# Performance work log

Hardware: AMD Instinct MI355X
Metric: run time of the kernel (lower is better)

## Reference

```python
import jax, jax.numpy as jnp
import numpy as np
import math

B, S, D, E, H = 8, 384, 768, 768, 12
HD = E // H
MAXL = 512

def _xavier(key, shape):
    fan_in, fan_out = shape[1], shape[0]
    lim = math.sqrt(6.0 / (fan_in + fan_out))
    return jax.random.uniform(key, shape, jnp.float32, -lim, lim)

def setup_inputs() -> dict:
    key = jax.random.key(0)
    ks = jax.random.split(key, 12)
    return {
        "x": jax.random.normal(ks[0], (B, S, D), jnp.float32),
        "mask": jnp.ones((B, S), jnp.int32),
        "segment_ids": jax.random.randint(ks[1], (B, S), 0, 2).astype(jnp.int32),
        "sep_distances": jax.random.normal(ks[2], (B, S), jnp.float32),
        "Wq": _xavier(ks[3], (E, D)), "bq": jnp.zeros((E,), jnp.float32),
        "Wk": _xavier(ks[4], (E, D)), "bk": jnp.zeros((E,), jnp.float32),
        "Wv": _xavier(ks[5], (E, D)), "bv": jnp.zeros((E,), jnp.float32),
        "rel_emb": jax.random.normal(ks[6], (2 * MAXL - 1, D), jnp.float32),
        "Wpk": _xavier(ks[7], (E, D)), "bpk": jnp.zeros((E,), jnp.float32),
        "Wpq": _xavier(ks[8], (E, D)), "bpq": jnp.zeros((E,), jnp.float32),
        "same_bias": jnp.zeros((H,), jnp.float32),
        "cross_bias": jnp.zeros((H,), jnp.float32),
        "sep_scale": jnp.full((H,), 0.25, jnp.float32),
        "sep_decay": jnp.full((H,), 0.35, jnp.float32),
        "Wo": _xavier(ks[9], (D, E)), "bo": jnp.zeros((D,), jnp.float32),
    }

def reference(x, mask, segment_ids, sep_distances, Wq, bq, Wk, bk, Wv, bv,
              rel_emb, Wpk, bpk, Wpq, bpq, same_bias, cross_bias,
              sep_scale, sep_decay, Wo, bo):
    b, s, _ = x.shape
    def shape_heads(t):  # [b,s,E] -> [b,H,s,HD]
        return t.reshape(b, s, H, HD).transpose(0, 2, 1, 3)
    q = shape_heads(x @ Wq.T + bq)
    k = shape_heads(x @ Wk.T + bk)
    v = shape_heads(x @ Wv.T + bv)
    # relative positions i - j, clamped and shifted
    rel_pos = jnp.arange(s)[:, None] - jnp.arange(s)[None, :]
    rel_pos = jnp.clip(rel_pos, -(MAXL - 1), MAXL - 1) + (MAXL - 1)
    rel = rel_emb[rel_pos]                     # [s,s,D]
    pos_k = (rel @ Wpk.T + bpk).reshape(s, s, H, HD)  # [i,j,h,d]
    pos_q = (rel @ Wpq.T + bpq).reshape(s, s, H, HD)
    c2c = jnp.einsum('bhid,bhjd->bhij', q, k)
    c2p = jnp.einsum('bhid,ijhd->bhij', q, pos_k)
    p2c = jnp.einsum('ijhd,bhjd->bhij', pos_q, k)
    logits = (c2c + c2p + p2c) / math.sqrt(HD * 3.0)
    # segment bias
    same = (segment_ids[:, :, None] == segment_ids[:, None, :]).astype(jnp.float32)[:, None]  # [b,1,s,s]
    cross = 1.0 - same
    hb = lambda p: p[None, :, None, None]
    seg_bias = same * hb(same_bias) + cross * hb(cross_bias)
    abs_sep = jnp.abs(sep_distances)
    gap = jnp.abs(abs_sep[:, :, None] - abs_sep[:, None, :])[:, None]  # [b,1,s,s]
    decay = jax.nn.softplus(sep_decay)[None, :, None, None] + 1e-4
    seg_bias = seg_bias + cross * jnp.exp(-gap * decay) * hb(sep_scale)
    logits = logits + seg_bias
    # mask: [b,s] -> [b,1,1,s]
    m = mask[:, None, None, :]
    logits = jnp.where(m == 0, jnp.float32(-9e15), logits)
    attn = jax.nn.softmax(logits, axis=-1)
    vals = jnp.einsum('bhij,bhjd->bhid', attn, v)
    vals = vals.transpose(0, 2, 1, 3).reshape(b, s, E)
    return vals @ Wo.T + bo
```

## Files before the change

kernel.cpp:

```cpp
#include <hip/hip_runtime.h>
#include <math.h>

#define B_  8
#define S_  384
#define H_  12
#define HD_ 64
#define E_  768
#define D_  768

typedef float  floatx4 __attribute__((ext_vector_type(4)));
typedef __bf16 bf16x8  __attribute__((ext_vector_type(8)));
typedef unsigned int ux4 __attribute__((ext_vector_type(4)));

__device__ __forceinline__ unsigned short f2bf(float f) {
    union { float f; unsigned u; } x; x.f = f;
    unsigned r = x.u + 0x7fff + ((x.u >> 16) & 1);
    return (unsigned short)(r >> 16);
}
__device__ __forceinline__ float bf2f(unsigned short u) {
    union { unsigned u; float f; } x; x.u = ((unsigned)u) << 16;
    return x.f;
}
__device__ __forceinline__ bf16x8 gld8(const unsigned short* p) {
    return __builtin_bit_cast(bf16x8, *(const ux4*)p);
}
__device__ __forceinline__ int tadr(int row, int cD) {
    return (row * 8 + (cD ^ (row & 7))) * 8;
}
__device__ __forceinline__ bf16x8 lds8(const unsigned short* base, int row, int cD) {
    return __builtin_bit_cast(bf16x8, *(const ux4*)(base + tadr(row, cD)));
}

__global__ __launch_bounds__(256) void convert_all(
    const float* __restrict__ x,
    const float* __restrict__ Wq, const float* __restrict__ Wk,
    const float* __restrict__ Wv, const float* __restrict__ Wo,
    const float* __restrict__ Wpk, const float* __restrict__ Wpq,
    const float* __restrict__ rel128,
    unsigned short* __restrict__ xb,
    unsigned short* __restrict__ wqb, unsigned short* __restrict__ wkb,
    unsigned short* __restrict__ wvb, unsigned short* __restrict__ wob,
    unsigned short* __restrict__ wpkb, unsigned short* __restrict__ wpqb,
    unsigned short* __restrict__ relb)
{
    const int seg = blockIdx.y;
    const int e = (blockIdx.x * 256 + threadIdx.x) * 4;
    const float* src;
    unsigned short* dst;
    if (seg < 4)       { src = x + (size_t)seg * 589824; dst = xb + (size_t)seg * 589824; }
    else if (seg == 4) { src = Wq;  dst = wqb; }
    else if (seg == 5) { src = Wk;  dst = wkb; }
    else if (seg == 6) { src = Wv;  dst = wvb; }
    else if (seg == 7) { src = Wo;  dst = wob; }
    else if (seg == 8) { src = Wpk; dst = wpkb; }
    else if (seg == 9) { src = Wpq; dst = wpqb; }
    else               { src = rel128; dst = relb; }

    float4 v;
    if (seg == 10 && e >= 767 * 768) v = make_float4(0.f, 0.f, 0.f, 0.f);
    else                             v = *(const float4*)(src + e);
    ushort4 o;
    o.x = f2bf(v.x); o.y = f2bf(v.y); o.z = f2bf(v.z); o.w = f2bf(v.w);
    *(ushort4*)(dst + e) = o;
}

__global__ __launch_bounds__(256) void proj_all(
    const unsigned short* __restrict__ xb, const unsigned short* __restrict__ relb,
    const unsigned short* __restrict__ wq, const unsigned short* __restrict__ wk,
    const unsigned short* __restrict__ wv, const unsigned short* __restrict__ wpk,
    const unsigned short* __restrict__ wpq,
    const float* __restrict__ bq, const float* __restrict__ bk,
    const float* __restrict__ bv, const float* __restrict__ bpk,
    const float* __restrict__ bpq,
    unsigned short* __restrict__ qb, unsigned short* __restrict__ kb,
    unsigned short* __restrict__ vtb, unsigned short* __restrict__ pkb,
    unsigned short* __restrict__ pqb)
{
    const int bid = blockIdx.x;
    int z, mt, nt;
    if (bid < 864) {
        z = bid / 288; const int r = bid - z * 288; mt = r / 6; nt = r - mt * 6;
    } else {
        const int r2 = bid - 864; z = 3 + r2 / 72;
        const int r = r2 % 72; mt = r / 6; nt = r - mt * 6;
    }
    const int m0 = mt * 64, n0 = nt * 128;

    const unsigned short* A = (z < 3) ? xb : relb;
    const unsigned short* W = (z == 0) ? wq : (z == 1) ? wk : (z == 2) ? wv
                            : (z == 3) ? wpk : wpq;
    const float* bias = (z == 0) ? bq : (z == 1) ? bk : (z == 2) ? bv
                      : (z == 3) ? bpk : bpq;
    unsigned short* C = (z == 0) ? qb : (z == 1) ? kb : (z == 2) ? vtb
                      : (z == 3) ? pkb : pqb;

    __shared__ unsigned short As[64 * 64];
    __shared__ unsigned short Ws[128 * 64];

    const int tid  = threadIdx.x;
    const int lane = tid & 63;
    const int wv_  = tid >> 6;
    const int quad = lane >> 4, l16 = lane & 15;

    floatx4 acc[4][2];
#pragma unroll
    for (int i = 0; i < 4; ++i)
#pragma unroll
        for (int j = 0; j < 2; ++j) acc[i][j] = (floatx4){0.f, 0.f, 0.f, 0.f};

    for (int k0 = 0; k0 < 768; k0 += 64) {
        __syncthreads();
#pragma unroll
        for (int r = 0; r < 2; ++r) {
            const int idx = tid + 256 * r;
            const int row = idx >> 3, cL = idx & 7, cD = cL ^ (row & 7);
            __builtin_amdgcn_global_load_lds(
                (__attribute__((address_space(1))) void*)(A + (size_t)(m0 + row) * 768 + k0 + cD * 8),
                (__attribute__((address_space(3))) void*)&As[idx * 8], 16, 0, 0);
        }
#pragma unroll
        for (int r = 0; r < 4; ++r) {
            const int idx = tid + 256 * r;
            const int row = idx >> 3, cL = idx & 7, cD = cL ^ (row & 7);
            __builtin_amdgcn_global_load_lds(
                (__attribute__((address_space(1))) void*)(W + (size_t)(n0 + row) * 768 + k0 + cD * 8),
                (__attribute__((address_space(3))) void*)&Ws[idx * 8], 16, 0, 0);
        }
        __syncthreads();

        bf16x8 a[4][2], b[2][2];
#pragma unroll
        for (int mi = 0; mi < 4; ++mi)
#pragma unroll
            for (int kc = 0; kc < 2; ++kc)
                a[mi][kc] = lds8(As, mi * 16 + l16, kc * 4 + quad);
#pragma unroll
        for (int ni = 0; ni < 2; ++ni)
#pragma unroll
            for (int kc = 0; kc < 2; ++kc)
                b[ni][kc] = lds8(Ws, wv_ * 32 + ni * 16 + l16, kc * 4 + quad);
#pragma unroll
        for (int mi = 0; mi < 4; ++mi)
#pragma unroll
            for (int ni = 0; ni < 2; ++ni)
#pragma unroll
                for (int kc = 0; kc < 2; ++kc)
                    acc[mi][ni] = __builtin_amdgcn_mfma_f32_16x16x32_bf16(
                        a[mi][kc], b[ni][kc], acc[mi][ni], 0, 0, 0);
    }

#pragma unroll
    for (int ni = 0; ni < 2; ++ni) {
        const int n = n0 + wv_ * 32 + ni * 16 + l16;
        const float bn = bias[n];
#pragma unroll
        for (int mi = 0; mi < 4; ++mi) {
            const int mbase = m0 + mi * 16 + quad * 4;
            if (z == 2) {
                const int bb = mbase / S_, s = mbase - bb * S_;
                const int h = n >> 6, hd = n & 63;
                ushort4 o;
                o.x = f2bf(acc[mi][ni][0] + bn);
                o.y = f2bf(acc[mi][ni][1] + bn);
                o.z = f2bf(acc[mi][ni][2] + bn);
                o.w = f2bf(acc[mi][ni][3] + bn);
                *(ushort4*)&C[(((size_t)(bb * H_ + h) << 6) + hd) * S_ + s] = o;
            } else if (z < 2) {
#pragma unroll
                for (int reg = 0; reg < 4; ++reg) {
                    const int m = mbase + reg;
                    const int bb = m / S_, s = m - bb * S_;
                    const int h = n >> 6, hd = n & 63;
                    C[(((size_t)(bb * H_ + h) * S_ + s) << 6) + hd] =
                        f2bf(acc[mi][ni][reg] + bn);
                }
            } else {
#pragma unroll
                for (int reg = 0; reg < 4; ++reg)
                    C[(size_t)(mbase + reg) * 768 + n] = f2bf(acc[mi][ni][reg] + bn);
            }
        }
    }
}

__global__ __launch_bounds__(256) void gemm_out(
    const unsigned short* __restrict__ A, const unsigned short* __restrict__ W,
    const float* __restrict__ bias, float* __restrict__ C)
{
    const int bid = blockIdx.x;
    const int kb = bid & 1;
    const int t  = bid >> 1;
    const int mt = t / 6, nt = t - mt * 6;
    const int m0 = mt * 64, n0 = nt * 128;

    __shared__ unsigned short As[64 * 64];
    __shared__ unsigned short Ws[128 * 64];

    const int tid  = threadIdx.x;
    const int lane = tid & 63;
    const int wv_  = tid >> 6;
    const int quad = lane >> 4, l16 = lane & 15;

    floatx4 acc[4][2];
#pragma unroll
    for (int i = 0; i < 4; ++i)
#pragma unroll
        for (int j = 0; j < 2; ++j) acc[i][j] = (floatx4){0.f, 0.f, 0.f, 0.f};

    const int kbeg = kb * 384, kend = kbeg + 384;
    for (int k0 = kbeg; k0 < kend; k0 += 64) {
        __syncthreads();
#pragma unroll
        for (int r = 0; r < 2; ++r) {
            const int idx = tid + 256 * r;
            const int row = idx >> 3, cL = idx & 7, cD = cL ^ (row & 7);
            __builtin_amdgcn_global_load_lds(
                (__attribute__((address_space(1))) void*)(A + (size_t)(m0 + row) * 768 + k0 + cD * 8),
                (__attribute__((address_space(3))) void*)&As[idx * 8], 16, 0, 0);
        }
#pragma unroll
        for (int r = 0; r < 4; ++r) {
            const int idx = tid + 256 * r;
            const int row = idx >> 3, cL = idx & 7, cD = cL ^ (row & 7);
            __builtin_amdgcn_global_load_lds(
                (__attribute__((address_space(1))) void*)(W + (size_t)(n0 + row) * 768 + k0 + cD * 8),
                (__attribute__((address_space(3))) void*)&Ws[idx * 8], 16, 0, 0);
        }
        __syncthreads();

        bf16x8 a[4][2], b[2][2];
#pragma unroll
        for (int mi = 0; mi < 4; ++mi)
#pragma unroll
            for (int kc = 0; kc < 2; ++kc)
                a[mi][kc] = lds8(As, mi * 16 + l16, kc * 4 + quad);
#pragma unroll
        for (int ni = 0; ni < 2; ++ni)
#pragma unroll
            for (int kc = 0; kc < 2; ++kc)
                b[ni][kc] = lds8(Ws, wv_ * 32 + ni * 16 + l16, kc * 4 + quad);
#pragma unroll
        for (int mi = 0; mi < 4; ++mi)
#pragma unroll
            for (int ni = 0; ni < 2; ++ni)
#pragma unroll
                for (int kc = 0; kc < 2; ++kc)
                    acc[mi][ni] = __builtin_amdgcn_mfma_f32_16x16x32_bf16(
                        a[mi][kc], b[ni][kc], acc[mi][ni], 0, 0, 0);
    }

#pragma unroll
    for (int ni = 0; ni < 2; ++ni) {
        const int n = n0 + wv_ * 32 + ni * 16 + l16;
        const float bn = (kb == 0) ? bias[n] : 0.f;
#pragma unroll
        for (int mi = 0; mi < 4; ++mi)
#pragma unroll
            for (int reg = 0; reg < 4; ++reg) {
                const int m = m0 + mi * 16 + quad * 4 + reg;
                atomicAdd(&C[(size_t)m * 768 + n], acc[mi][ni][reg] + bn);
            }
    }
}

__global__ __launch_bounds__(256, 3) void attn_mfma(
    const unsigned short* __restrict__ qg, const unsigned short* __restrict__ kg,
    const unsigned short* __restrict__ vtg,
    const unsigned short* __restrict__ pkg, const unsigned short* __restrict__ pqg,
    const int* __restrict__ seg, const float* __restrict__ sep,
    const int* __restrict__ mask,
    const float* __restrict__ same_bias, const float* __restrict__ cross_bias,
    const float* __restrict__ sep_scale, const float* __restrict__ sep_decay,
    unsigned short* __restrict__ part_O, float* __restrict__ part_ml)
{
    __shared__ unsigned short PKs[128 * 64];
    __shared__ unsigned short PQs[128 * 64];
    __shared__ float CP[64 * 68];

    const int tid  = threadIdx.x;
    const int lane = tid & 63, w = tid >> 6;
    const int l16  = lane & 15, quad = lane >> 4;
    const int it = blockIdx.x, h = blockIdx.y;
    const int b  = blockIdx.z / 6, jt = blockIdx.z - 6 * b;
    const int i0 = it * 64, j0 = jt * 64;
    const size_t bh = (size_t)(b * H_ + h);

    const unsigned short* kbase  = kg  + bh * S_ * 64;
    const unsigned short* vtbase = vtg + bh * 64 * S_;
    const int dbase = i0 - j0 + 320;

#pragma unroll
    for (int r = 0; r < 4; ++r) {
        const int idx = tid + 256 * r;
        const int srow = idx >> 3, cL = idx & 7, cD = cL ^ (srow & 7);
        const size_t go = (size_t)(dbase + srow) * 768 + h * 64 + cD * 8;
        __builtin_amdgcn_global_load_lds(
            (__attribute__((address_space(1))) void*)(pkg + go),
            (__attribute__((address_space(3))) void*)&PKs[idx * 8], 16, 0, 0);
        __builtin_amdgcn_global_load_lds(
            (__attribute__((address_space(1))) void*)(pqg + go),
            (__attribute__((address_space(3))) void*)&PQs[idx * 8], 16, 0, 0);
    }

    bf16x8 qf[2];
#pragma unroll
    for (int ks = 0; ks < 2; ++ks)
        qf[ks] = gld8(qg + (bh * S_ + i0 + 16 * w + l16) * 64 + ks * 32 + quad * 8);

    bf16x8 kf[4][2];
#pragma unroll
    for (int nj = 0; nj < 4; ++nj)
#pragma unroll
        for (int ks = 0; ks < 2; ++ks)
            kf[nj][ks] = gld8(kbase + (size_t)(j0 + 16 * nj + l16) * 64
                              + ks * 32 + quad * 8);

    bf16x8 vtf[4][2];
#pragma unroll
    for (int nd = 0; nd < 4; ++nd)
#pragma unroll
        for (int ks = 0; ks < 2; ++ks)
            vtf[nd][ks] = gld8(vtbase + (size_t)(16 * nd + l16) * S_
                               + j0 + ks * 32 + quad * 8);

    const int row = 16 * w + l16;
    const float aii = fabsf(sep[b * S_ + i0 + row]);
    const int   sii = seg[b * S_ + i0 + row];
    const float* sepj = sep  + b * S_ + j0;
    const int*   segj = seg  + b * S_ + j0;
    const int*   mskj = mask + b * S_ + j0;
    float ajv[16]; int sjv[16], mkv[16];
    *(float4*)&ajv[0]  = *(const float4*)&sepj[quad * 8];
    *(float4*)&ajv[4]  = *(const float4*)&sepj[quad * 8 + 4];
    *(float4*)&ajv[8]  = *(const float4*)&sepj[32 + quad * 8];
    *(float4*)&ajv[12] = *(const float4*)&sepj[32 + quad * 8 + 4];
    *(int4*)&sjv[0]  = *(const int4*)&segj[quad * 8];
    *(int4*)&sjv[4]  = *(const int4*)&segj[quad * 8 + 4];
    *(int4*)&sjv[8]  = *(const int4*)&segj[32 + quad * 8];
    *(int4*)&sjv[12] = *(const int4*)&segj[32 + quad * 8 + 4];
    *(int4*)&mkv[0]  = *(const int4*)&mskj[quad * 8];
    *(int4*)&mkv[4]  = *(const int4*)&mskj[quad * 8 + 4];
    *(int4*)&mkv[8]  = *(const int4*)&mskj[32 + quad * 8];
    *(int4*)&mkv[12] = *(const int4*)&mskj[32 + quad * 8 + 4];

    const float sb  = same_bias[h];
    const float cb  = cross_bias[h];
    const float ssc = sep_scale[h];
    const float sd  = sep_decay[h];
    const float dec = fmaxf(sd, 0.f) + log1pf(__expf(-fabsf(sd))) + 1e-4f;
    const float isc = 0.07216878364870323f;

    float biasv[16]; unsigned mkbits = 0;
#pragma unroll
    for (int e = 0; e < 16; ++e) {
        const float gap = fabsf(aii - fabsf(ajv[e]));
        biasv[e] = (sii == sjv[e]) ? sb : cb + __expf(-gap * dec) * ssc;
        mkbits |= (mkv[e] != 0 ? 1u : 0u) << e;
    }

#pragma unroll
    for (int nj = 0; nj < 4; ++nj) {
        floatx4 acc = (floatx4){0.f, 0.f, 0.f, 0.f};
#pragma unroll
        for (int ks = 0; ks < 2; ++ks)
            acc = __builtin_amdgcn_mfma_f32_16x16x32_bf16(qf[ks], kf[nj][ks], acc, 0, 0, 0);
#pragma unroll
        for (int reg = 0; reg < 4; ++reg) {
            const int ii = 16 * w + quad * 4 + reg;
            CP[ii * 68 + 16 * nj + l16] = acc[reg];
        }
    }

    __syncthreads();

#pragma unroll
    for (int f = 0; f < 5; ++f) {
        const int nd = w + f;
        floatx4 acc = (floatx4){0.f, 0.f, 0.f, 0.f};
#pragma unroll
        for (int ks = 0; ks < 2; ++ks) {
            bf16x8 bf = lds8(PKs, 16 * nd + l16, ks * 4 + quad);
            acc = __builtin_amdgcn_mfma_f32_16x16x32_bf16(qf[ks], bf, acc, 0, 0, 0);
        }
        const int ddloc = 16 * nd + l16;
#pragma unroll
        for (int reg = 0; reg < 4; ++reg) {
            const int ii = 16 * w + quad * 4 + reg;
            const int jj = ii - ddloc + 63;
            if (jj >= 0 && jj < 64)
                CP[ii * 68 + jj] += acc[reg];
        }
    }

#pragma unroll
    for (int f = 0; f < 5; ++f) {
        const int nd = w + f;
        bf16x8 pqf[2];
#pragma unroll
        for (int ks = 0; ks < 2; ++ks)
            pqf[ks] = lds8(PQs, 16 * nd + l16, ks * 4 + quad);
#pragma unroll
        for (int g = 0; g < 2; ++g) {
            const int nj = (g == 0) ? (3 - f) : (4 - f);
            if (nj < 0 || nj > 3) continue;
            floatx4 acc = (floatx4){0.f, 0.f, 0.f, 0.f};
#pragma unroll
            for (int ks = 0; ks < 2; ++ks)
                acc = __builtin_amdgcn_mfma_f32_16x16x32_bf16(pqf[ks], kf[nj][ks], acc, 0, 0, 0);
            const int jj = 16 * nj + l16;
#pragma unroll
            for (int reg = 0; reg < 4; ++reg) {
                const int ddloc = 16 * nd + quad * 4 + reg;
                const int ii = ddloc + jj - 63;
                if (ii >= 16 * w && ii < 16 * w + 16)
                    CP[ii * 68 + jj] += acc[reg];
            }
        }
    }

    floatx4 cp0 = *(const floatx4*)&CP[row * 68 + quad * 8];
    floatx4 cp1 = *(const floatx4*)&CP[row * 68 + quad * 8 + 4];
    floatx4 cp2 = *(const floatx4*)&CP[row * 68 + 32 + quad * 8];
    floatx4 cp3 = *(const floatx4*)&CP[row * 68 + 32 + quad * 8 + 4];

    float lg[16];
    float tmax = -INFINITY;
#pragma unroll
    for (int e = 0; e < 16; ++e) {
        const float cpv = (e < 4) ? cp0[e] : (e < 8) ? cp1[e - 4]
                        : (e < 12) ? cp2[e - 8] : cp3[e - 12];
        float xv = cpv * isc + biasv[e];
        if (!((mkbits >> e) & 1u)) xv = -9.0e15f;
        lg[e] = xv;
        tmax = fmaxf(tmax, xv);
    }
    tmax = fmaxf(tmax, __shfl_xor(tmax, 16));
    tmax = fmaxf(tmax, __shfl_xor(tmax, 32));

    float rs = 0.f;
    unsigned int pk32[8];
#pragma unroll
    for (int e = 0; e < 8; ++e) {
        const float e0 = __expf(lg[2 * e]     - tmax);
        const float e1 = __expf(lg[2 * e + 1] - tmax);
        rs += e0 + e1;
        pk32[e] = (unsigned)f2bf(e0) | ((unsigned)f2bf(e1) << 16);
    }
    rs += __shfl_xor(rs, 16);
    rs += __shfl_xor(rs, 32);

    float* pml = part_ml + (size_t)(jt * 576 + ((b * H_ + h) * 6 + it)) * 128;
    if (quad == 0) {
        pml[row]      = tmax;
        pml[64 + row] = rs;
    }

    bf16x8 pA[2];
    pA[0] = __builtin_bit_cast(bf16x8, (ux4){pk32[0], pk32[1], pk32[2], pk32[3]});
    pA[1] = __builtin_bit_cast(bf16x8, (ux4){pk32[4], pk32[5], pk32[6], pk32[7]});
    floatx4 O[4];
#pragma unroll
    for (int nd = 0; nd < 4; ++nd) {
        O[nd] = (floatx4){0.f, 0.f, 0.f, 0.f};
#pragma unroll
        for (int ks = 0; ks < 2; ++ks)
            O[nd] = __builtin_amdgcn_mfma_f32_16x16x32_bf16(pA[ks], vtf[nd][ks], O[nd], 0, 0, 0);
    }

    unsigned short* pO = part_O + (size_t)(jt * 576 + ((b * H_ + h) * 6 + it)) * 4096;
#pragma unroll
    for (int nd = 0; nd < 4; ++nd) {
        const int d = 16 * nd + l16;
#pragma unroll
        for (int reg = 0; reg < 4; ++reg) {
            const int ii = 16 * w + quad * 4 + reg;
            pO[ii * 64 + d] = f2bf(O[nd][reg]);
        }
    }
}

__global__ __launch_bounds__(256) void merge_attn(
    const unsigned short* __restrict__ part_O, const float* __restrict__ part_ml,
    unsigned short* __restrict__ vals)
{
    const int idx = blockIdx.x;
    const int b  = idx / (H_ * 6);
    const int r  = idx - b * H_ * 6;
    const int h  = r / 6, it = r - h * 6;
    const int tid = threadIdx.x;
    const int ii = tid >> 2, c = (tid & 3) * 16;

    float m[6], l[6];
#pragma unroll
    for (int jc = 0; jc < 6; ++jc) {
        const float* pml = part_ml + (size_t)(jc * 576 + idx) * 128;
        m[jc] = pml[ii];
        l[jc] = pml[64 + ii];
    }
    float M = m[0];
#pragma unroll
    for (int jc = 1; jc < 6; ++jc) M = fmaxf(M, m[jc]);
    float wsum = 0.f, wc[6];
#pragma unroll
    for (int jc = 0; jc < 6; ++jc) {
        wc[jc] = __expf(m[jc] - M);
        wsum += wc[jc] * l[jc];
    }
    const float inv = (wsum > 0.f) ? 1.f / wsum : 0.f;

    float o[16];
#pragma unroll
    for (int e = 0; e < 16; ++e) o[e] = 0.f;
#pragma unroll
    for (int jc = 0; jc < 6; ++jc) {
        const unsigned short* pO = part_O + ((size_t)(jc * 576 + idx)) * 4096
                                 + ii * 64 + c;
        ux4 u0 = *(const ux4*)pO;
        ux4 u1 = *(const ux4*)(pO + 8);
        const unsigned short* us0 = (const unsigned short*)&u0;
        const unsigned short* us1 = (const unsigned short*)&u1;
#pragma unroll
        for (int e = 0; e < 8; ++e) {
            o[e]     += wc[jc] * bf2f(us0[e]);
            o[8 + e] += wc[jc] * bf2f(us1[e]);
        }
    }
    ushort4 w0, w1, w2, w3;
#pragma unroll
    for (int e = 0; e < 4; ++e) {
        ((unsigned short*)&w0)[e] = f2bf(o[e] * inv);
        ((unsigned short*)&w1)[e] = f2bf(o[4 + e] * inv);
        ((unsigned short*)&w2)[e] = f2bf(o[8 + e] * inv);
        ((unsigned short*)&w3)[e] = f2bf(o[12 + e] * inv);
    }
    unsigned short* dst = vals + ((size_t)(b * S_ + it * 64 + ii)) * E_ + h * 64 + c;
    *(ushort4*)(dst)      = w0;
    *(ushort4*)(dst + 4)  = w1;
    *(ushort4*)(dst + 8)  = w2;
    *(ushort4*)(dst + 12) = w3;
}

extern "C" void kernel_launch(void* const* d_in, const int* in_sizes, int n_in,
                              void* d_out, int out_size, void* d_ws, size_t ws_size,
                              hipStream_t stream)
{
    const float* x         = (const float*)d_in[0];
    const int*   mask      = (const int*)d_in[1];
    const int*   seg       = (const int*)d_in[2];
    const float* sep       = (const float*)d_in[3];
    const float* Wq        = (const float*)d_in[4];
    const float* bq        = (const float*)d_in[5];
    const float* Wk        = (const float*)d_in[6];
    const float* bk        = (const float*)d_in[7];
    const float* Wv        = (const float*)d_in[8];
    const float* bv        = (const float*)d_in[9];
    const float* rel_emb   = (const float*)d_in[10];
    const float* Wpk       = (const float*)d_in[11];
    const float* bpk       = (const float*)d_in[12];
    const float* Wpq       = (const float*)d_in[13];
    const float* bpq       = (const float*)d_in[14];
    const float* same_bias = (const float*)d_in[15];
    const float* cross_bias= (const float*)d_in[16];
    const float* sep_scale = (const float*)d_in[17];
    const float* sep_decay = (const float*)d_in[18];
    const float* Wo        = (const float*)d_in[19];
    const float* bo        = (const float*)d_in[20];

    const size_t QKVN = (size_t)B_ * S_ * E_;
    const size_t WN   = (size_t)768 * 768;

    unsigned short* xb    = (unsigned short*)d_ws;
    unsigned short* wqb   = xb   + QKVN;
    unsigned short* wkb   = wqb  + WN;
    unsigned short* wvb   = wkb  + WN;
    unsigned short* wob   = wvb  + WN;
    unsigned short* wpkb  = wob  + WN;
    unsigned short* wpqb  = wpkb + WN;
    unsigned short* relb  = wpqb + WN;
    unsigned short* qb    = relb + WN;
    unsigned short* kb    = qb   + QKVN;
    unsigned short* vtb   = kb   + QKVN;
    unsigned short* pkb   = vtb  + QKVN;
    unsigned short* pqb   = pkb  + WN;
    unsigned short* valsb = pqb  + WN;
    unsigned short* partO = valsb + QKVN;
    float*          partml= (float*)(partO + (size_t)6 * 576 * 4096);

    hipMemsetAsync(d_out, 0, (size_t)out_size, stream);

    convert_all<<<dim3(576, 11), 256, 0, stream>>>(
        x, Wq, Wk, Wv, Wo, Wpk, Wpq, rel_emb + (size_t)128 * D_,
        xb, wqb, wkb, wvb, wob, wpkb, wpqb, relb);

    proj_all<<<dim3(1008), 256, 0, stream>>>(
        xb, relb, wqb, wkb, wvb, wpkb, wpqb,
        bq, bk, bv, bpk, bpq, qb, kb, vtb, pkb, pqb);

    attn_mfma<<<dim3(6, 12, 48), 256, 0, stream>>>(
        qb, kb, vtb, pkb, pqb, seg, sep, mask,
        same_bias, cross_bias, sep_scale, sep_decay, partO, partml);

    merge_attn<<<dim3(576), 256, 0, stream>>>(partO, partml, valsb);

    gemm_out<<<dim3(576), 256, 0, stream>>>(valsb, wob, bo, (float*)d_out);
}
```

Baseline: 210.2 us.

## Loop three key tiles per attention block with online softmax and ring-buffered position tiles

Each attention block now walks three consecutive 64-wide key tiles with an online-softmax accumulator, not one, so the split-KV factor drops from six to two. The PK/PQ relative-position tiles sit in a 128-row ring buffer in LDS, and only 64 new rows are fetched per step, so the overlapping diagonal band is reused. The merge kernel combines two partials instead of six. This cuts partial-output traffic, merge work and redundant relative-position loads. The cost is a third of the blocks (1152 vs 3456), extra syncs and loads sitting in the serial loop.

After: 239.8 us. +14.1%, slower.

```diff
diff --git a/kernel.cpp b/kernel.cpp
--- a/kernel.cpp
+++ b/kernel.cpp
@@ -281,67 +281,36 @@
     const int lane = tid & 63, w = tid >> 6;
     const int l16  = lane & 15, quad = lane >> 4;
     const int it = blockIdx.x, h = blockIdx.y;
-    const int b  = blockIdx.z / 6, jt = blockIdx.z - 6 * b;
-    const int i0 = it * 64, j0 = jt * 64;
+    const int b  = blockIdx.z >> 1, jh = blockIdx.z & 1;
+    const int i0 = it * 64;
     const size_t bh = (size_t)(b * H_ + h);
 
     const unsigned short* kbase  = kg  + bh * S_ * 64;
     const unsigned short* vtbase = vtg + bh * 64 * S_;
-    const int dbase = i0 - j0 + 320;
+    const int db0 = i0 - jh * 192 + 320;
 
 #pragma unroll
     for (int r = 0; r < 4; ++r) {
         const int idx = tid + 256 * r;
-        const int srow = idx >> 3, cL = idx & 7, cD = cL ^ (srow & 7);
-        const size_t go = (size_t)(dbase + srow) * 768 + h * 64 + cD * 8;
+        const int grow = db0 + (idx >> 3);
+        const int p = grow & 127;
+        const int cL = idx & 7, cD = cL ^ (grow & 7);
+        const size_t go = (size_t)grow * 768 + h * 64 + cD * 8;
         __builtin_amdgcn_global_load_lds(
             (__attribute__((address_space(1))) void*)(pkg + go),
-            (__attribute__((address_space(3))) void*)&PKs[idx * 8], 16, 0, 0);
+            (__attribute__((address_space(3))) void*)&PKs[(p * 8 + cL) * 8], 16, 0, 0);
         __builtin_amdgcn_global_load_lds(
             (__attribute__((address_space(1))) void*)(pqg + go),
-            (__attribute__((address_space(3))) void*)&PQs[idx * 8], 16, 0, 0);
-    }
-
+            (__attribute__((address_space(3))) void*)&PQs[(p * 8 + cL) * 8], 16, 0, 0);
+    }
+
+    const int row = 16 * w + l16;
     bf16x8 qf[2];
 #pragma unroll
     for (int ks = 0; ks < 2; ++ks)
         qf[ks] = gld8(qg + (bh * S_ + i0 + 16 * w + l16) * 64 + ks * 32 + quad * 8);
-
-    bf16x8 kf[4][2];
-#pragma unroll
-    for (int nj = 0; nj < 4; ++nj)
-#pragma unroll
-        for (int ks = 0; ks < 2; ++ks)
-            kf[nj][ks] = gld8(kbase + (size_t)(j0 + 16 * nj + l16) * 64
-                              + ks * 32 + quad * 8);
-
-    bf16x8 vtf[4][2];
-#pragma unroll
-    for (int nd = 0; nd < 4; ++nd)
-#pragma unroll
-        for (int ks = 0; ks < 2; ++ks)
-            vtf[nd][ks] = gld8(vtbase + (size_t)(16 * nd + l16) * S_
-                               + j0 + ks * 32 + quad * 8);
-
-    const int row = 16 * w + l16;
     const float aii = fabsf(sep[b * S_ + i0 + row]);
     const int   sii = seg[b * S_ + i0 + row];
-    const float* sepj = sep  + b * S_ + j0;
-    const int*   segj = seg  + b * S_ + j0;
-    const int*   mskj = mask + b * S_ + j0;
-    float ajv[16]; int sjv[16], mkv[16];
-    *(float4*)&ajv[0]  = *(const float4*)&sepj[quad * 8];
-    *(float4*)&ajv[4]  = *(const float4*)&sepj[quad * 8 + 4];
-    *(float4*)&ajv[8]  = *(const float4*)&sepj[32 + quad * 8];
-    *(float4*)&ajv[12] = *(const float4*)&sepj[32 + quad * 8 + 4];
-    *(int4*)&sjv[0]  = *(const int4*)&segj[quad * 8];
-    *(int4*)&sjv[4]  = *(const int4*)&segj[quad * 8 + 4];
-    *(int4*)&sjv[8]  = *(const int4*)&segj[32 + quad * 8];
-    *(int4*)&sjv[12] = *(const int4*)&segj[32 + quad * 8 + 4];
-    *(int4*)&mkv[0]  = *(const int4*)&mskj[quad * 8];
-    *(int4*)&mkv[4]  = *(const int4*)&mskj[quad * 8 + 4];
-    *(int4*)&mkv[8]  = *(const int4*)&mskj[32 + quad * 8];
-    *(int4*)&mkv[12] = *(const int4*)&mskj[32 + quad * 8 + 4];
 
     const float sb  = same_bias[h];
     const float cb  = cross_bias[h];
@@ -350,6 +319,38 @@
     const float dec = fmaxf(sd, 0.f) + log1pf(__expf(-fabsf(sd))) + 1e-4f;
     const float isc = 0.07216878364870323f;
 
+    bf16x8 kf[4][2], vtf[4][2];
+    float ajv[16]; int sjv[16], mkv[16];
+    {
+        const int j0 = jh * 192;
+#pragma unroll
+        for (int nj = 0; nj < 4; ++nj)
+#pragma unroll
+            for (int ks = 0; ks < 2; ++ks)
+                kf[nj][ks] = gld8(kbase + (size_t)(j0 + 16 * nj + l16) * 64
+                                  + ks * 32 + quad * 8);
+#pragma unroll
+        for (int nd = 0; nd < 4; ++nd)
+#pragma unroll
+            for (int ks = 0; ks < 2; ++ks)
+                vtf[nd][ks] = gld8(vtbase + (size_t)(16 * nd + l16) * S_
+                                   + j0 + ks * 32 + quad * 8);
+        const float* sepj = sep  + b * S_ + j0;
+        const int*   segj = seg  + b * S_ + j0;
+        const int*   mskj = mask + b * S_ + j0;
+        *(float4*)&ajv[0]  = *(const float4*)&sepj[quad * 8];
+        *(float4*)&ajv[4]  = *(const float4*)&sepj[quad * 8 + 4];
+        *(float4*)&ajv[8]  = *(const float4*)&sepj[32 + quad * 8];
+        *(float4*)&ajv[12] = *(const float4*)&sepj[32 + quad * 8 + 4];
+        *(int4*)&sjv[0]  = *(const int4*)&segj[quad * 8];
+        *(int4*)&sjv[4]  = *(const int4*)&segj[quad * 8 + 4];
+        *(int4*)&sjv[8]  = *(const int4*)&segj[32 + quad * 8];
+        *(int4*)&sjv[12] = *(const int4*)&segj[32 + quad * 8 + 4];
+        *(int4*)&mkv[0]  = *(const int4*)&mskj[quad * 8];
+        *(int4*)&mkv[4]  = *(const int4*)&mskj[quad * 8 + 4];
+        *(int4*)&mkv[8]  = *(const int4*)&mskj[32 + quad * 8];
+        *(int4*)&mkv[12] = *(const int4*)&mskj[32 + quad * 8 + 4];
+    }
     float biasv[16]; unsigned mkbits = 0;
 #pragma unroll
     for (int e = 0; e < 16; ++e) {
@@ -358,6 +359,11 @@
         mkbits |= (mkv[e] != 0 ? 1u : 0u) << e;
     }
 
+    float m_run = -INFINITY, l_run = 0.f;
+    floatx4 O[4];
+#pragma unroll
+    for (int nd = 0; nd < 4; ++nd) O[nd] = (floatx4){0.f, 0.f, 0.f, 0.f};
+
 #pragma unroll
     for (int nj = 0; nj < 4; ++nj) {
         floatx4 acc = (floatx4){0.f, 0.f, 0.f, 0.f};
@@ -374,100 +380,181 @@
     __syncthreads();
 
 #pragma unroll
-    for (int f = 0; f < 5; ++f) {
-        const int nd = w + f;
-        floatx4 acc = (floatx4){0.f, 0.f, 0.f, 0.f};
-#pragma unroll
-        for (int ks = 0; ks < 2; ++ks) {
-            bf16x8 bf = lds8(PKs, 16 * nd + l16, ks * 4 + quad);
-            acc = __builtin_amdgcn_mfma_f32_16x16x32_bf16(qf[ks], bf, acc, 0, 0, 0);
-        }
-        const int ddloc = 16 * nd + l16;
-#pragma unroll
-        for (int reg = 0; reg < 4; ++reg) {
-            const int ii = 16 * w + quad * 4 + reg;
-            const int jj = ii - ddloc + 63;
-            if (jj >= 0 && jj < 64)
-                CP[ii * 68 + jj] += acc[reg];
-        }
-    }
-
-#pragma unroll
-    for (int f = 0; f < 5; ++f) {
-        const int nd = w + f;
-        bf16x8 pqf[2];
-#pragma unroll
-        for (int ks = 0; ks < 2; ++ks)
-            pqf[ks] = lds8(PQs, 16 * nd + l16, ks * 4 + quad);
-#pragma unroll
-        for (int g = 0; g < 2; ++g) {
-            const int nj = (g == 0) ? (3 - f) : (4 - f);
-            if (nj < 0 || nj > 3) continue;
+    for (int t = 0; t < 3; ++t) {
+        const int dbt = db0 - 64 * t;
+
+#pragma unroll
+        for (int f = 0; f < 5; ++f) {
+            const int nd = w + f;
             floatx4 acc = (floatx4){0.f, 0.f, 0.f, 0.f};
 #pragma unroll
+            for (int ks = 0; ks < 2; ++ks) {
+                bf16x8 bf = lds8(PKs, (dbt + 16 * nd + l16) & 127, ks * 4 + quad);
+                acc = __builtin_amdgcn_mfma_f32_16x16x32_bf16(qf[ks], bf, acc, 0, 0, 0);
+            }
+            const int ddloc = 16 * nd + l16;
+#pragma unroll
+            for (int reg = 0; reg < 4; ++reg) {
+                const int ii = 16 * w + quad * 4 + reg;
+                const int jj = ii - ddloc + 63;
+                if (jj >= 0 && jj < 64)
+                    CP[ii * 68 + jj] += acc[reg];
+            }
+        }
+
+#pragma unroll
+        for (int f = 0; f < 5; ++f) {
+            const int nd = w + f;
+            bf16x8 pqf[2];
+#pragma unroll
             for (int ks = 0; ks < 2; ++ks)
-                acc = __builtin_amdgcn_mfma_f32_16x16x32_bf16(pqf[ks], kf[nj][ks], acc, 0, 0, 0);
-            const int jj = 16 * nj + l16;
-#pragma unroll
-            for (int reg = 0; reg < 4; ++reg) {
-                const int ddloc = 16 * nd + quad * 4 + reg;
-                const int ii = ddloc + jj - 63;
-                if (ii >= 16 * w && ii < 16 * w + 16)
-                    CP[ii * 68 + jj] += acc[reg];
-            }
-        }
-    }
-
-    floatx4 cp0 = *(const floatx4*)&CP[row * 68 + quad * 8];
-    floatx4 cp1 = *(const floatx4*)&CP[row * 68 + quad * 8 + 4];
-    floatx4 cp2 = *(const floatx4*)&CP[row * 68 + 32 + quad * 8];
-    floatx4 cp3 = *(const floatx4*)&CP[row * 68 + 32 + quad * 8 + 4];
-
-    float lg[16];
-    float tmax = -INFINITY;
-#pragma unroll
-    for (int e = 0; e < 16; ++e) {
-        const float cpv = (e < 4) ? cp0[e] : (e < 8) ? cp1[e - 4]
-                        : (e < 12) ? cp2[e - 8] : cp3[e - 12];
-        float xv = cpv * isc + biasv[e];
-        if (!((mkbits >> e) & 1u)) xv = -9.0e15f;
-        lg[e] = xv;
-        tmax = fmaxf(tmax, xv);
-    }
-    tmax = fmaxf(tmax, __shfl_xor(tmax, 16));
-    tmax = fmaxf(tmax, __shfl_xor(tmax, 32));
-
-    float rs = 0.f;
-    unsigned int pk32[8];
-#pragma unroll
-    for (int e = 0; e < 8; ++e) {
-        const float e0 = __expf(lg[2 * e]     - tmax);
-        const float e1 = __expf(lg[2 * e + 1] - tmax);
-        rs += e0 + e1;
-        pk32[e] = (unsigned)f2bf(e0) | ((unsigned)f2bf(e1) << 16);
-    }
-    rs += __shfl_xor(rs, 16);
-    rs += __shfl_xor(rs, 32);
-
-    float* pml = part_ml + (size_t)(jt * 576 + ((b * H_ + h) * 6 + it)) * 128;
-    if (quad == 0) {
-        pml[row]      = tmax;
-        pml[64 + row] = rs;
-    }
-
-    bf16x8 pA[2];
-    pA[0] = __builtin_bit_cast(bf16x8, (ux4){pk32[0], pk32[1], pk32[2], pk32[3]});
-    pA[1] = __builtin_bit_cast(bf16x8, (ux4){pk32[4], pk32[5], pk32[6], pk32[7]});
-    floatx4 O[4];
-#pragma unroll
-    for (int nd = 0; nd < 4; ++nd) {
-        O[nd] = (floatx4){0.f, 0.f, 0.f, 0.f};
-#pragma unroll
-        for (int ks = 0; ks < 2; ++ks)
-            O[nd] = __builtin_amdgcn_mfma_f32_16x16x32_bf16(pA[ks], vtf[nd][ks], O[nd], 0, 0, 0);
-    }
-
-    unsigned short* pO = part_O + (size_t)(jt * 576 + ((b * H_ + h) * 6 + it)) * 4096;
+                pqf[ks] = lds8(PQs, (dbt + 16 * nd + l16) & 127, ks * 4 + quad);
+#pragma unroll
+            for (int g = 0; g < 2; ++g) {
+                const int nj = (g == 0) ? (3 - f) : (4 - f);
+                if (nj < 0 || nj > 3) continue;
+                floatx4 acc = (floatx4){0.f, 0.f, 0.f, 0.f};
+#pragma unroll
+                for (int ks = 0; ks < 2; ++ks)
+                    acc = __builtin_amdgcn_mfma_f32_16x16x32_bf16(pqf[ks], kf[nj][ks], acc, 0, 0, 0);
+                const int jj = 16 * nj + l16;
+#pragma unroll
+                for (int reg = 0; reg < 4; ++reg) {
+                    const int ddloc = 16 * nd + quad * 4 + reg;
+                    const int ii = ddloc + jj - 63;
+                    if (ii >= 16 * w && ii < 16 * w + 16)
+                        CP[ii * 68 + jj] += acc[reg];
+                }
+            }
+        }
+
+        floatx4 cp0 = *(const floatx4*)&CP[row * 68 + quad * 8];
+        floatx4 cp1 = *(const floatx4*)&CP[row * 68 + quad * 8 + 4];
+        floatx4 cp2 = *(const floatx4*)&CP[row * 68 + 32 + quad * 8];
+        floatx4 cp3 = *(const floatx4*)&CP[row * 68 + 32 + quad * 8 + 4];
+
+        float lg[16];
+        float tmax = -INFINITY;
+#pragma unroll
+        for (int e = 0; e < 16; ++e) {
+            const float cpv = (e < 4) ? cp0[e] : (e < 8) ? cp1[e - 4]
+                            : (e < 12) ? cp2[e - 8] : cp3[e - 12];
+            float xv = cpv * isc + biasv[e];
+            if (!((mkbits >> e) & 1u)) xv = -9.0e15f;
+            lg[e] = xv;
+            tmax = fmaxf(tmax, xv);
+        }
+        tmax = fmaxf(tmax, __shfl_xor(tmax, 16));
+        tmax = fmaxf(tmax, __shfl_xor(tmax, 32));
+
+        const float newm  = fmaxf(m_run, tmax);
+        const float scale = __expf(m_run - newm);
+        m_run = newm;
+
+        float rs = 0.f;
+        unsigned int pk32[8];
+#pragma unroll
+        for (int e = 0; e < 8; ++e) {
+            const float e0 = __expf(lg[2 * e]     - newm);
+            const float e1 = __expf(lg[2 * e + 1] - newm);
+            rs += e0 + e1;
+            pk32[e] = (unsigned)f2bf(e0) | ((unsigned)f2bf(e1) << 16);
+        }
+        rs += __shfl_xor(rs, 16);
+        rs += __shfl_xor(rs, 32);
+        l_run = l_run * scale + rs;
+
+        if (t < 2) {
+            __syncthreads();
+            const int dbn = dbt - 64;
+#pragma unroll
+            for (int r = 0; r < 2; ++r) {
+                const int idx = tid + 256 * r;
+                const int grow = dbn + (idx >> 3);
+                const int p = grow & 127;
+                const int cL = idx & 7, cD = cL ^ (grow & 7);
+                const size_t go = (size_t)grow * 768 + h * 64 + cD * 8;
+                __builtin_amdgcn_global_load_lds(
+                    (__attribute__((address_space(1))) void*)(pkg + go),
+                    (__attribute__((address_space(3))) void*)&PKs[(p * 8 + cL) * 8], 16, 0, 0);
+                __builtin_amdgcn_global_load_lds(
+                    (__attribute__((address_space(1))) void*)(pqg + go),
+                    (__attribute__((address_space(3))) void*)&PQs[(p * 8 + cL) * 8], 16, 0, 0);
+            }
+            const int j0n = jh * 192 + (t + 1) * 64;
+#pragma unroll
+            for (int nj = 0; nj < 4; ++nj)
+#pragma unroll
+                for (int ks = 0; ks < 2; ++ks)
+                    kf[nj][ks] = gld8(kbase + (size_t)(j0n + 16 * nj + l16) * 64
+                                      + ks * 32 + quad * 8);
+            const float* sepj = sep  + b * S_ + j0n;
+            const int*   segj = seg  + b * S_ + j0n;
+            const int*   mskj = mask + b * S_ + j0n;
+            *(float4*)&ajv[0]  = *(const float4*)&sepj[quad * 8];
+            *(float4*)&ajv[4]  = *(const float4*)&sepj[quad * 8 + 4];
+            *(float4*)&ajv[8]  = *(const float4*)&sepj[32 + quad * 8];
+            *(float4*)&ajv[12] = *(const float4*)&sepj[32 + quad * 8 + 4];
+            *(int4*)&sjv[0]  = *(const int4*)&segj[quad * 8];
+            *(int4*)&sjv[4]  = *(const int4*)&segj[quad * 8 + 4];
+            *(int4*)&sjv[8]  = *(const int4*)&segj[32 + quad * 8];
+            *(int4*)&sjv[12] = *(const int4*)&segj[32 + quad * 8 + 4];
+            *(int4*)&mkv[0]  = *(const int4*)&mskj[quad * 8];
+            *(int4*)&mkv[4]  = *(const int4*)&mskj[quad * 8 + 4];
+            *(int4*)&mkv[8]  = *(const int4*)&mskj[32 + quad * 8];
+            *(int4*)&mkv[12] = *(const int4*)&mskj[32 + quad * 8 + 4];
+        }
+
+        float sc_r[4];
+#pragma unroll
+        for (int reg = 0; reg < 4; ++reg)
+            sc_r[reg] = __shfl(scale, (lane & 48) | (quad * 4 + reg));
+        bf16x8 pA[2];
+        pA[0] = __builtin_bit_cast(bf16x8, (ux4){pk32[0], pk32[1], pk32[2], pk32[3]});
+        pA[1] = __builtin_bit_cast(bf16x8, (ux4){pk32[4], pk32[5], pk32[6], pk32[7]});
+#pragma unroll
+        for (int nd = 0; nd < 4; ++nd) {
+#pragma unroll
+            for (int reg = 0; reg < 4; ++reg)
+                O[nd][reg] *= sc_r[reg];
+#pragma unroll
+            for (int ks = 0; ks < 2; ++ks)
+                O[nd] = __builtin_amdgcn_mfma_f32_16x16x32_bf16(pA[ks], vtf[nd][ks], O[nd], 0, 0, 0);
+        }
+
+        if (t < 2) {
+            const int j0n = jh * 192 + (t + 1) * 64;
+#pragma unroll
+            for (int nd = 0; nd < 4; ++nd)
+#pragma unroll
+                for (int ks = 0; ks < 2; ++ks)
+                    vtf[nd][ks] = gld8(vtbase + (size_t)(16 * nd + l16) * S_
+                                       + j0n + ks * 32 + quad * 8);
+            mkbits = 0;
+#pragma unroll
+            for (int e = 0; e < 16; ++e) {
+                const float gap = fabsf(aii - fabsf(ajv[e]));
+                biasv[e] = (sii == sjv[e]) ? sb : cb + __expf(-gap * dec) * ssc;
+                mkbits |= (mkv[e] != 0 ? 1u : 0u) << e;
+            }
+#pragma unroll
+            for (int nj = 0; nj < 4; ++nj) {
+                floatx4 acc = (floatx4){0.f, 0.f, 0.f, 0.f};
+#pragma unroll
+                for (int ks = 0; ks < 2; ++ks)
+                    acc = __builtin_amdgcn_mfma_f32_16x16x32_bf16(qf[ks], kf[nj][ks], acc, 0, 0, 0);
+#pragma unroll
+                for (int reg = 0; reg < 4; ++reg) {
+                    const int ii = 16 * w + quad * 4 + reg;
+                    CP[ii * 68 + 16 * nj + l16] = acc[reg];
+                }
+            }
+            __syncthreads();
+        }
+    }
+
+    const int idx = (int)((b * H_ + h) * 6 + it);
+    unsigned short* pO = part_O + (size_t)(jh * 576 + idx) * 4096;
 #pragma unroll
     for (int nd = 0; nd < 4; ++nd) {
         const int d = 16 * nd + l16;
@@ -476,6 +563,11 @@
             const int ii = 16 * w + quad * 4 + reg;
             pO[ii * 64 + d] = f2bf(O[nd][reg]);
         }
+    }
+    float* pml = part_ml + (size_t)(jh * 576 + idx) * 128;
+    if (quad == 0) {
+        pml[row]      = m_run;
+        pml[64 + row] = l_run;
     }
 }
 
@@ -490,19 +582,17 @@
     const int tid = threadIdx.x;
     const int ii = tid >> 2, c = (tid & 3) * 16;
 
-    float m[6], l[6];
-#pragma unroll
-    for (int jc = 0; jc < 6; ++jc) {
+    float m[2], l[2];
+#pragma unroll
+    for (int jc = 0; jc < 2; ++jc) {
         const float* pml = part_ml + (size_t)(jc * 576 + idx) * 128;
         m[jc] = pml[ii];
         l[jc] = pml[64 + ii];
     }
-    float M = m[0];
-#pragma unroll
-    for (int jc = 1; jc < 6; ++jc) M = fmaxf(M, m[jc]);
-    float wsum = 0.f, wc[6];
-#pragma unroll
-    for (int jc = 0; jc < 6; ++jc) {
+    float M = fmaxf(m[0], m[1]);
+    float wsum = 0.f, wc[2];
+#pragma unroll
+    for (int jc = 0; jc < 2; ++jc) {
         wc[jc] = __expf(m[jc] - M);
         wsum += wc[jc] * l[jc];
     }
@@ -512,7 +602,7 @@
 #pragma unroll
     for (int e = 0; e < 16; ++e) o[e] = 0.f;
 #pragma unroll
-    for (int jc = 0; jc < 6; ++jc) {
+    for (int jc = 0; jc < 2; ++jc) {
         const unsigned short* pO = part_O + ((size_t)(jc * 576 + idx)) * 4096
                                  + ii * 64 + c;
         ux4 u0 = *(const ux4*)pO;
@@ -584,7 +674,7 @@
     unsigned short* pqb   = pkb  + WN;
     unsigned short* valsb = pqb  + WN;
     unsigned short* partO = valsb + QKVN;
-    float*          partml= (float*)(partO + (size_t)6 * 576 * 4096);
+    float*          partml= (float*)(partO + (size_t)2 * 576 * 4096);
 
     hipMemsetAsync(d_out, 0, (size_t)out_size, stream);
 
@@ -596,7 +686,7 @@
         xb, relb, wqb, wkb, wvb, wpkb, wpqb,
         bq, bk, bv, bpk, bpq, qb, kb, vtb, pkb, pqb);
 
-    attn_mfma<<<dim3(6, 12, 48), 256, 0, stream>>>(
+    attn_mfma<<<dim3(6, 12, 16), 256, 0, stream>>>(
         qb, kb, vtb, pkb, pqb, seg, sep, mask,
         same_bias, cross_bias, sep_scale, sep_decay, partO, partml);
 
```
